# Optimization experiments

Hardware: AMD Instinct MI355X
Metric: run time of the kernel (lower is better)

Reference implementation:

```python
import jax, jax.numpy as jnp
import numpy as np

EPS = 1e-5  # BatchNorm eps

def gcn_conv(x, src, dst, deg, dinv, W, b):
    # PyG GCNConv: out = D^{-1/2}(A+I)D^{-1/2} X W + b
    N = x.shape[0]
    xw = x @ W                               # [N, F_out]
    norm = dinv[src] * dinv[dst]             # [E]
    agg = jax.ops.segment_sum(xw[src] * norm[:, None], dst, num_segments=N)
    agg = agg + xw * (1.0 / deg)[:, None]    # self-loop term: deg^-1/2 * deg^-1/2
    return agg + b

def bn(x, g, b, m, v):
    # inference-mode BatchNorm1d over features
    return (x - m) * jax.lax.rsqrt(v + EPS) * g + b

def setup_inputs() -> dict:
    key = jax.random.key(0)
    N, E, F_in, C = 100000, 1600000, 128, 16
    dims = [F_in, 64, 128, 64, 32, C]
    ks = jax.random.split(key, 64)
    inp = {}
    inp["x"] = jax.random.normal(ks[0], (N, F_in), dtype=jnp.float32)
    inp["edge_index"] = jax.random.randint(ks[1], (2, E), 0, N, dtype=jnp.int32)
    ki = 2
    for l in range(5):
        fi, fo = dims[l], dims[l + 1]
        scale = 1.0 / np.sqrt(fi)
        inp[f"w{l+1}"] = jax.random.normal(ks[ki], (fi, fo), dtype=jnp.float32) * scale; ki += 1
        inp[f"b{l+1}"] = jnp.zeros((fo,), dtype=jnp.float32)
    for l in range(4):  # BN params for layers 1..4
        fo = dims[l + 1]
        inp[f"g{l+1}"] = jnp.ones((fo,), dtype=jnp.float32)
        inp[f"be{l+1}"] = jnp.zeros((fo,), dtype=jnp.float32)
        inp[f"m{l+1}"] = jax.random.normal(ks[ki], (fo,), dtype=jnp.float32) * 0.1; ki += 1
        inp[f"v{l+1}"] = jax.random.uniform(ks[ki], (fo,), dtype=jnp.float32, minval=0.5, maxval=1.5); ki += 1
    return inp

def reference(x, edge_index,
              w1, b1, w2, b2, w3, b3, w4, b4, w5, b5,
              g1, be1, m1, v1, g2, be2, m2, v2,
              g3, be3, m3, v3, g4, be4, m4, v4):
    N = x.shape[0]
    src, dst = edge_index[0], edge_index[1]
    deg = jax.ops.segment_sum(jnp.ones(src.shape[0], x.dtype), dst, num_segments=N) + 1.0
    dinv = jax.lax.rsqrt(deg)
    h = jax.nn.relu(bn(gcn_conv(x, src, dst, deg, dinv, w1, b1), g1, be1, m1, v1))
    h = jax.nn.relu(bn(gcn_conv(h, src, dst, deg, dinv, w2, b2), g2, be2, m2, v2))
    h = jax.nn.relu(bn(gcn_conv(h, src, dst, deg, dinv, w3, b3), g3, be3, m3, v3))
    h = jax.nn.relu(bn(gcn_conv(h, src, dst, deg, dinv, w4, b4), g4, be4, m4, v4))
    return gcn_conv(h, src, dst, deg, dinv, w5, b5)
```

## Files before the change

kernel.cpp:

```cpp
#include <hip/hip_runtime.h>
#include <hip/hip_fp16.h>

#define BEPS 1e-5f
static constexpr int TPB = 256;
static constexpr int G_SC = 512;
static constexpr int BK_SHIFT = 8;
static constexpr int BK_NODES = 256;
static constexpr int KMAX = 512;

union F4H8 { float4 f4; __half2 h2[4]; };

typedef _Float16 half8 __attribute__((ext_vector_type(8)));
typedef float floatx4 __attribute__((ext_vector_type(4)));


__global__ __launch_bounds__(TPB) void k_zero_int(int* __restrict__ p, int n) {
  int i = blockIdx.x * TPB + threadIdx.x;
  if (i < n) p[i] = 0;
}

__global__ __launch_bounds__(TPB) void k_hist(const int* __restrict__ dst,
                                              int* __restrict__ histG,
                                              int* __restrict__ btot,
                                              int E, int K, int chunk) {
  __shared__ int lh[KMAX];
  int g = blockIdx.x, t = threadIdx.x;
  for (int i = t; i < KMAX; i += TPB) lh[i] = 0;
  __syncthreads();
  int e0 = g * chunk, e1 = min(E, e0 + chunk);
  for (int e = e0 + t; e < e1; e += TPB) atomicAdd(&lh[dst[e] >> BK_SHIFT], 1);
  __syncthreads();
  for (int i = t; i < K; i += TPB) {
    histG[i * G_SC + g] = lh[i];
    atomicAdd(&btot[i], lh[i]);
  }
}

__global__ __launch_bounds__(KMAX) void k_bbase(const int* __restrict__ btot,
                                                int* __restrict__ bbase, int K) {
  __shared__ int sh[KMAX];
  int t = threadIdx.x;
  int v = (t < K) ? btot[t] : 0;
  sh[t] = v;
  __syncthreads();
  for (int s = 1; s < KMAX; s <<= 1) {
    int x = sh[t];
    int y = (t >= s) ? sh[t - s] : 0;
    __syncthreads();
    sh[t] = x + y;
    __syncthreads();
  }
  if (t < K) bbase[t] = sh[t] - v;
  if (t == 0) bbase[K] = sh[K - 1];
}

__global__ __launch_bounds__(G_SC) void k_offs(const int* __restrict__ histG,
                                               const int* __restrict__ bbase,
                                               int* __restrict__ offs) {
  __shared__ int sh[G_SC];
  int b = blockIdx.x, t = threadIdx.x;
  int v = histG[b * G_SC + t];
  sh[t] = v;
  __syncthreads();
  for (int s = 1; s < G_SC; s <<= 1) {
    int x = sh[t];
    int y = (t >= s) ? sh[t - s] : 0;
    __syncthreads();
    sh[t] = x + y;
    __syncthreads();
  }
  offs[b * G_SC + t] = bbase[b] + sh[t] - v;
}

__global__ __launch_bounds__(TPB) void k_scatter(const int* __restrict__ src,
                                                 const int* __restrict__ dst,
                                                 const int* __restrict__ offs,
                                                 unsigned int* __restrict__ pairs,
                                                 int E, int K, int chunk) {
  __shared__ int cur[KMAX];
  int g = blockIdx.x, t = threadIdx.x;
  for (int i = t; i < K; i += TPB) cur[i] = offs[i * G_SC + g];
  __syncthreads();
  int e0 = g * chunk, e1 = min(E, e0 + chunk);
  for (int e = e0 + t; e < e1; e += TPB) {
    int d = dst[e];
    int b = d >> BK_SHIFT;
    int pos = atomicAdd(&cur[b], 1);
    pairs[pos] = (unsigned int)src[e] | ((unsigned int)(d & (BK_NODES - 1)) << 20);
  }
}

__global__ __launch_bounds__(TPB) void k_bucket_sort(const unsigned int* __restrict__ pairs,
                                                     const int* __restrict__ bbase,
                                                     int* __restrict__ rowptr,
                                                     int* __restrict__ colidx,
                                                     float* __restrict__ dinv,
                                                     int N, int E) {
  __shared__ int deg[BK_NODES];
  __shared__ int sh[BK_NODES];
  int b = blockIdx.x, t = threadIdx.x;
  int base = bbase[b], end = bbase[b + 1];
  int n0 = b << BK_SHIFT;
  int nNodes = min(BK_NODES, N - n0);
  deg[t] = 0;
  __syncthreads();
  for (int e = base + t; e < end; e += TPB) atomicAdd(&deg[pairs[e] >> 20], 1);
  __syncthreads();
  int v = deg[t];
  sh[t] = v;
  __syncthreads();
  for (int s = 1; s < TPB; s <<= 1) {
    int x = sh[t];
    int y = (t >= s) ? sh[t - s] : 0;
    __syncthreads();
    sh[t] = x + y;
    __syncthreads();
  }
  int excl = sh[t] - v;
  if (t < nNodes) {
    rowptr[n0 + t] = base + excl;
    dinv[n0 + t] = rsqrtf((float)(v + 1));
  }
  if (b == (int)gridDim.x - 1 && t == 0) rowptr[N] = E;
  __syncthreads();
  deg[t] = excl;
  __syncthreads();
  for (int e = base + t; e < end; e += TPB) {
    unsigned int p = pairs[e];
    int pos = atomicAdd(&deg[p >> 20], 1);
    colidx[base + pos] = (int)(p & 0xFFFFFu);
  }
}

__global__ __launch_bounds__(TPB) void k_packW(const float* __restrict__ W,
                                               _Float16* __restrict__ Wp,
                                               int K, int FO) {
  int i = blockIdx.x * TPB + threadIdx.x;
  if (i >= K * FO) return;
  int j = i & 7;
  int lane = (i >> 3) & 63;
  int tile = i >> 9;
  int nct = FO >> 4;
  int ct = tile % nct, kch = tile / nct;
  int k = kch * 32 + ((lane >> 4) << 3) + j;
  int n = (ct << 4) + (lane & 15);
  Wp[i] = (_Float16)W[k * FO + n];
}

template <int FI, int FO, int EPI, bool F32IN>
__global__ __launch_bounds__(TPB) void k_mgemm(const void* __restrict__ hin,
                                               const _Float16* __restrict__ Wp,
                                               const float* __restrict__ dinv,
                                               const float* __restrict__ bias,
                                               const float* __restrict__ g,
                                               const float* __restrict__ be,
                                               const float* __restrict__ m,
                                               const float* __restrict__ v,
                                               __half* __restrict__ out, int N) {
  constexpr int NCT = FO / 16;
  constexpr int NKC = FI / 32;
  __shared__ float4 Wsh[NKC * NCT * 64];
  for (int i = threadIdx.x; i < NKC * NCT * 64; i += TPB)
    Wsh[i] = reinterpret_cast<const float4*>(Wp)[i];
  __syncthreads();

  int lane = threadIdx.x & 63;
  int wv = threadIdx.x >> 6;
  int quad = lane >> 4;
  int rowBase = blockIdx.x * 64 + wv * 16;
  int rA = min(rowBase + (lane & 15), N - 1);

  floatx4 acc[NCT];
#pragma unroll
  for (int ct = 0; ct < NCT; ++ct) acc[ct] = (floatx4){0.f, 0.f, 0.f, 0.f};

#pragma unroll
  for (int kch = 0; kch < NKC; ++kch) {
    half8 a;
    if constexpr (F32IN) {
      const float4* xp = reinterpret_cast<const float4*>(hin);
      size_t idx = ((size_t)rA * FI + kch * 32 + quad * 8) >> 2;
      float4 fa = xp[idx], fb = xp[idx + 1];
      a[0] = (_Float16)fa.x; a[1] = (_Float16)fa.y; a[2] = (_Float16)fa.z; a[3] = (_Float16)fa.w;
      a[4] = (_Float16)fb.x; a[5] = (_Float16)fb.y; a[6] = (_Float16)fb.z; a[7] = (_Float16)fb.w;
    } else {
      union { float4 f4; half8 h8; } ua;
      ua.f4 = reinterpret_cast<const float4*>(hin)[((size_t)rA * FI + kch * 32 + quad * 8) >> 3];
      a = ua.h8;
    }
#pragma unroll
    for (int ct = 0; ct < NCT; ++ct) {
      union { float4 f4; half8 h8; } ub;
      ub.f4 = Wsh[(kch * NCT + ct) * 64 + lane];
      acc[ct] = __builtin_amdgcn_mfma_f32_16x16x32_f16(a, ub.h8, acc[ct], 0, 0, 0);
    }
  }

  int r0 = rowBase + quad * 4;
  if (EPI == 0) {
    float dv[4];
#pragma unroll
    for (int reg = 0; reg < 4; ++reg) dv[reg] = (r0 + reg < N) ? dinv[r0 + reg] : 0.f;
#pragma unroll
    for (int ct = 0; ct < NCT; ++ct) {
      int col = ct * 16 + (lane & 15);
#pragma unroll
      for (int reg = 0; reg < 4; ++reg) {
        int r = r0 + reg;
        if (r < N) out[(size_t)r * FO + col] = __float2half(acc[ct][reg] * dv[reg]);
      }
    }
  } else {
#pragma unroll
    for (int ct = 0; ct < NCT; ++ct) {
      int col = ct * 16 + (lane & 15);
      float sc = g[col] * rsqrtf(v[col] + BEPS);
      float bb = bias[col] - m[col];
      float ee = be[col];
#pragma unroll
      for (int reg = 0; reg < 4; ++reg) {
        int r = r0 + reg;
        if (r < N) out[(size_t)r * FO + col] = __float2half(fmaxf((acc[ct][reg] + bb) * sc + ee, 0.f));
      }
    }
  }
}

template <int F, int MODE, typename TO>
__global__ __launch_bounds__(TPB) void k_agg(const __half* __restrict__ in,
                                             const int* __restrict__ rowptr,
                                             const int* __restrict__ colidx,
                                             const float* __restrict__ dinv,
                                             const float* __restrict__ bias,
                                             const float* __restrict__ g,
                                             const float* __restrict__ be,
                                             const float* __restrict__ m,
                                             const float* __restrict__ v,
                                             TO* __restrict__ out, int N) {
  constexpr int V = F / 8;
  constexpr int NPB = TPB / V;
  int node = blockIdx.x * NPB + (int)(threadIdx.x / V);
  int lane = threadIdx.x % V;
  if (node >= N) return;
  const float4* in16 = reinterpret_cast<const float4*>(in);
  const size_t rs = F / 8;
  float acc[8];
  {
    F4H8 u;
    u.f4 = in16[(size_t)node * rs + lane];
#pragma unroll
    for (int i = 0; i < 4; ++i) {
      float2 t2 = __half22float2(u.h2[i]);
      acc[2 * i] = t2.x;
      acc[2 * i + 1] = t2.y;
    }
  }
  int e0 = rowptr[node], e1 = rowptr[node + 1];
  int e = e0;
  for (; e + 4 <= e1; e += 4) {
    int s0 = colidx[e + 0], s1 = colidx[e + 1], s2 = colidx[e + 2], s3 = colidx[e + 3];
    F4H8 u0, u1, u2, u3;
    u0.f4 = in16[(size_t)s0 * rs + lane];
    u1.f4 = in16[(size_t)s1 * rs + lane];
    u2.f4 = in16[(size_t)s2 * rs + lane];
    u3.f4 = in16[(size_t)s3 * rs + lane];
#pragma unroll
    for (int i = 0; i < 4; ++i) {
      float2 a = __half22float2(u0.h2[i]), b = __half22float2(u1.h2[i]);
      float2 c = __half22float2(u2.h2[i]), d = __half22float2(u3.h2[i]);
      acc[2 * i] += (a.x + b.x) + (c.x + d.x);
      acc[2 * i + 1] += (a.y + b.y) + (c.y + d.y);
    }
  }
  for (; e < e1; ++e) {
    F4H8 u;
    u.f4 = in16[(size_t)colidx[e] * rs + lane];
#pragma unroll
    for (int i = 0; i < 4; ++i) {
      float2 t2 = __half22float2(u.h2[i]);
      acc[2 * i] += t2.x;
      acc[2 * i + 1] += t2.y;
    }
  }
  float dv = dinv[node];
#pragma unroll
  for (int i = 0; i < 8; ++i) acc[i] *= dv;
  if (MODE == 0) {
    float4 ba = reinterpret_cast<const float4*>(bias)[lane * 2];
    float4 bb = reinterpret_cast<const float4*>(bias)[lane * 2 + 1];
    acc[0] += ba.x; acc[1] += ba.y; acc[2] += ba.z; acc[3] += ba.w;
    acc[4] += bb.x; acc[5] += bb.y; acc[6] += bb.z; acc[7] += bb.w;
  } else if (MODE == 1 || MODE == 2) {
    const float4* B = reinterpret_cast<const float4*>(bias);
    const float4* G = reinterpret_cast<const float4*>(g);
    const float4* Be = reinterpret_cast<const float4*>(be);
    const float4* M = reinterpret_cast<const float4*>(m);
    const float4* Vv = reinterpret_cast<const float4*>(v);
#pragma unroll
    for (int h = 0; h < 2; ++h) {
      float4 b4 = B[lane * 2 + h], g4 = G[lane * 2 + h], e4 = Be[lane * 2 + h];
      float4 m4 = M[lane * 2 + h], v4 = Vv[lane * 2 + h];
      float* a = acc + 4 * h;
      a[0] = fmaxf((a[0] + b4.x - m4.x) * (g4.x * rsqrtf(v4.x + BEPS)) + e4.x, 0.f);
      a[1] = fmaxf((a[1] + b4.y - m4.y) * (g4.y * rsqrtf(v4.y + BEPS)) + e4.y, 0.f);
      a[2] = fmaxf((a[2] + b4.z - m4.z) * (g4.z * rsqrtf(v4.z + BEPS)) + e4.z, 0.f);
      a[3] = fmaxf((a[3] + b4.w - m4.w) * (g4.w * rsqrtf(v4.w + BEPS)) + e4.w, 0.f);
    }
    if (MODE == 2) {
#pragma unroll
      for (int i = 0; i < 8; ++i) acc[i] *= dv;
    }
  }
  if constexpr (sizeof(TO) == 2) {
    F4H8 u;
#pragma unroll
    for (int i = 0; i < 4; ++i) u.h2[i] = __floats2half2_rn(acc[2 * i], acc[2 * i + 1]);
    reinterpret_cast<float4*>(out)[(size_t)node * rs + lane] = u.f4;
  } else {
    float4 o0 = {acc[0], acc[1], acc[2], acc[3]};
    float4 o1 = {acc[4], acc[5], acc[6], acc[7]};
    float4* op = reinterpret_cast<float4*>((float*)out + (size_t)node * F + lane * 8);
    op[0] = o0;
    op[1] = o1;
  }
}


extern "C" void kernel_launch(void* const* d_in, const int* in_sizes, int n_in,
                              void* d_out, int out_size, void* d_ws, size_t ws_size,
                              hipStream_t stream) {
  const float* x = (const float*)d_in[0];
  const int* ei = (const int*)d_in[1];
  const int N = in_sizes[0] / 128;
  const int E = in_sizes[1] / 2;
  const int* src = ei;
  const int* dst = ei + E;

  const float* w1 = (const float*)d_in[2];  const float* b1 = (const float*)d_in[3];
  const float* w2 = (const float*)d_in[4];  const float* b2 = (const float*)d_in[5];
  const float* w3 = (const float*)d_in[6];  const float* b3 = (const float*)d_in[7];
  const float* w4 = (const float*)d_in[8];  const float* b4 = (const float*)d_in[9];
  const float* w5 = (const float*)d_in[10]; const float* b5 = (const float*)d_in[11];
  const float* g1 = (const float*)d_in[12]; const float* be1 = (const float*)d_in[13];
  const float* m1 = (const float*)d_in[14]; const float* v1 = (const float*)d_in[15];
  const float* g2 = (const float*)d_in[16]; const float* be2 = (const float*)d_in[17];
  const float* m2 = (const float*)d_in[18]; const float* v2 = (const float*)d_in[19];
  const float* g3 = (const float*)d_in[20]; const float* be3 = (const float*)d_in[21];
  const float* m3 = (const float*)d_in[22]; const float* v3 = (const float*)d_in[23];
  const float* g4 = (const float*)d_in[24]; const float* be4 = (const float*)d_in[25];
  const float* m4 = (const float*)d_in[26]; const float* v4 = (const float*)d_in[27];
  float* out = (float*)d_out;

  char* ws = (char*)d_ws;
  size_t off = 0;
  auto alloc = [&](size_t bytes) -> void* {
    void* p = ws + off;
    off += (bytes + 255) & ~(size_t)255;
    return p;
  };
  float*        dinv   = (float*)alloc((size_t)N * 4);
  int*          rowptr = (int*)alloc((size_t)(N + 1) * 4);
  int*          colidx = (int*)alloc((size_t)E * 4);
  unsigned int* pairs  = (unsigned int*)alloc((size_t)E * 4);
  int*          histG  = (int*)alloc((size_t)KMAX * G_SC * 4);
  int*          offs   = (int*)alloc((size_t)KMAX * G_SC * 4);
  int*          btot   = (int*)alloc(KMAX * 4);
  int*          bbase  = (int*)alloc((KMAX + 1) * 4);
  _Float16*     wp1    = (_Float16*)alloc(128 * 64 * 2);
  _Float16*     wp2    = (_Float16*)alloc(64 * 128 * 2);
  _Float16*     wp3    = (_Float16*)alloc(128 * 64 * 2);
  _Float16*     wp4    = (_Float16*)alloc(64 * 32 * 2);
  _Float16*     wp5    = (_Float16*)alloc(32 * 16 * 2);
  __half*       bufA   = (__half*)alloc((size_t)N * 128 * 2);
  __half*       bufB   = (__half*)alloc((size_t)N * 128 * 2);
  (void)ws_size; (void)n_in; (void)out_size;

  const int K = (N + BK_NODES - 1) >> BK_SHIFT;
  const int chunk = (E + G_SC - 1) / G_SC;

  k_zero_int<<<2, TPB, 0, stream>>>(btot, KMAX);
  k_hist<<<G_SC, TPB, 0, stream>>>(dst, histG, btot, E, K, chunk);
  k_bbase<<<1, KMAX, 0, stream>>>(btot, bbase, K);
  k_offs<<<K, G_SC, 0, stream>>>(histG, bbase, offs);
  k_scatter<<<G_SC, TPB, 0, stream>>>(src, dst, offs, pairs, E, K, chunk);
  k_bucket_sort<<<K, TPB, 0, stream>>>(pairs, bbase, rowptr, colidx, dinv, N, E);

  k_packW<<<(128 * 64 + TPB - 1) / TPB, TPB, 0, stream>>>(w1, wp1, 128, 64);
  k_packW<<<(64 * 128 + TPB - 1) / TPB, TPB, 0, stream>>>(w2, wp2, 64, 128);
  k_packW<<<(128 * 64 + TPB - 1) / TPB, TPB, 0, stream>>>(w3, wp3, 128, 64);
  k_packW<<<(64 * 32 + TPB - 1) / TPB, TPB, 0, stream>>>(w4, wp4, 64, 32);
  k_packW<<<(32 * 16 + TPB - 1) / TPB, TPB, 0, stream>>>(w5, wp5, 32, 16);

  int gRow = (N + 63) / 64;
  k_mgemm<128, 64, 0, true><<<gRow, TPB, 0, stream>>>(x, wp1, dinv, nullptr, nullptr, nullptr, nullptr, nullptr, bufB, N);
  k_agg<64, 2, __half><<<(N + 31) / 32, TPB, 0, stream>>>(bufB, rowptr, colidx, dinv, b1, g1, be1, m1, v1, bufA, N);
  k_agg<64, 3, __half><<<(N + 31) / 32, TPB, 0, stream>>>(bufA, rowptr, colidx, dinv, nullptr, nullptr, nullptr, nullptr, nullptr, bufB, N);
  k_mgemm<64, 128, 1, false><<<gRow, TPB, 0, stream>>>(bufB, wp2, nullptr, b2, g2, be2, m2, v2, bufA, N);
  k_mgemm<128, 64, 0, false><<<gRow, TPB, 0, stream>>>(bufA, wp3, dinv, nullptr, nullptr, nullptr, nullptr, nullptr, bufB, N);
  k_agg<64, 1, __half><<<(N + 31) / 32, TPB, 0, stream>>>(bufB, rowptr, colidx, dinv, b3, g3, be3, m3, v3, bufA, N);
  k_mgemm<64, 32, 0, false><<<gRow, TPB, 0, stream>>>(bufA, wp4, dinv, nullptr, nullptr, nullptr, nullptr, nullptr, bufB, N);
  k_agg<32, 1, __half><<<(N + 63) / 64, TPB, 0, stream>>>(bufB, rowptr, colidx, dinv, b4, g4, be4, m4, v4, bufA, N);
  k_mgemm<32, 16, 0, false><<<gRow, TPB, 0, stream>>>(bufA, wp5, dinv, nullptr, nullptr, nullptr, nullptr, nullptr, bufB, N);
  k_agg<16, 0, float><<<(N + 127) / 128, TPB, 0, stream>>>(bufB, rowptr, colidx, dinv, b5, nullptr, nullptr, nullptr, nullptr, out, N);
}
```

Measured before the change: 389.6 us.

## Process aggregation nodes in degree-sorted order, unroll gathers by eight, merge weight packing

A degree histogram is built during CSR construction and counting-sorted into a node permutation. The permutation runs highest degree first, so each wavefront in the aggregation kernels handles nodes with similar neighbor counts and waits less on its slowest node. The aggregation loop also gains an 8-way unrolled gather to keep more loads in flight. The five weight-packing launches are merged into one. In exchange there are two extra small kernels, and per-node reads and writes follow a permuted, scattered order that loses locality.

```diff
diff --git a/kernel.cpp b/kernel.cpp
--- a/kernel.cpp
+++ b/kernel.cpp
@@ -95,6 +95,7 @@
                                                      int* __restrict__ rowptr,
                                                      int* __restrict__ colidx,
                                                      float* __restrict__ dinv,
+                                                     int* __restrict__ dhist,
                                                      int N, int E) {
   __shared__ int deg[BK_NODES];
   __shared__ int sh[BK_NODES];
@@ -120,6 +121,7 @@
   if (t < nNodes) {
     rowptr[n0 + t] = base + excl;
     dinv[n0 + t] = rsqrtf((float)(v + 1));
+    atomicAdd(&dhist[min(v, 63)], 1);
   }
   if (b == (int)gridDim.x - 1 && t == 0) rowptr[N] = E;
   __syncthreads();
@@ -132,19 +134,50 @@
   }
 }
 
-__global__ __launch_bounds__(TPB) void k_packW(const float* __restrict__ W,
-                                               _Float16* __restrict__ Wp,
-                                               int K, int FO) {
+__global__ __launch_bounds__(64) void k_degbase(const int* __restrict__ dhist,
+                                                int* __restrict__ dcur) {
+  __shared__ int sh[64];
+  int t = threadIdx.x;
+  sh[t] = dhist[t];
+  __syncthreads();
+  if (t == 0) {
+    int acc = 0;
+    for (int d = 63; d >= 0; --d) { int c = sh[d]; sh[d] = acc; acc += c; }
+  }
+  __syncthreads();
+  dcur[t] = sh[t];
+}
+
+__global__ __launch_bounds__(TPB) void k_degscatter(const int* __restrict__ rowptr,
+                                                    int* __restrict__ dcur,
+                                                    int* __restrict__ order, int N) {
   int i = blockIdx.x * TPB + threadIdx.x;
-  if (i >= K * FO) return;
-  int j = i & 7;
-  int lane = (i >> 3) & 63;
-  int tile = i >> 9;
-  int nct = FO >> 4;
-  int ct = tile % nct, kch = tile / nct;
+  if (i >= N) return;
+  int d = min(rowptr[i + 1] - rowptr[i], 63);
+  int pos = atomicAdd(&dcur[d], 1);
+  order[pos] = i;
+}
+
+__device__ inline void packone(const float* __restrict__ W, _Float16* __restrict__ Wp,
+                               int i, int FO) {
+  int j = i & 7, lane = (i >> 3) & 63, tile = i >> 9;
+  int nct = FO >> 4, ct = tile % nct, kch = tile / nct;
   int k = kch * 32 + ((lane >> 4) << 3) + j;
   int n = (ct << 4) + (lane & 15);
   Wp[i] = (_Float16)W[k * FO + n];
+}
+
+__global__ __launch_bounds__(TPB) void k_packAll(const float* w1, _Float16* p1,
+                                                 const float* w2, _Float16* p2,
+                                                 const float* w3, _Float16* p3,
+                                                 const float* w4, _Float16* p4,
+                                                 const float* w5, _Float16* p5) {
+  int i = blockIdx.x * TPB + threadIdx.x;
+  if (i < 8192) packone(w1, p1, i, 64);
+  else if (i < 16384) packone(w2, p2, i - 8192, 128);
+  else if (i < 24576) packone(w3, p3, i - 16384, 64);
+  else if (i < 26624) packone(w4, p4, i - 24576, 32);
+  else if (i < 27136) packone(w5, p5, i - 26624, 16);
 }
 
 template <int FI, int FO, int EPI, bool F32IN>
@@ -230,6 +263,7 @@
 __global__ __launch_bounds__(TPB) void k_agg(const __half* __restrict__ in,
                                              const int* __restrict__ rowptr,
                                              const int* __restrict__ colidx,
+                                             const int* __restrict__ order,
                                              const float* __restrict__ dinv,
                                              const float* __restrict__ bias,
                                              const float* __restrict__ g,
@@ -239,9 +273,10 @@
                                              TO* __restrict__ out, int N) {
   constexpr int V = F / 8;
   constexpr int NPB = TPB / V;
-  int node = blockIdx.x * NPB + (int)(threadIdx.x / V);
+  int gidx = blockIdx.x * NPB + (int)(threadIdx.x / V);
   int lane = threadIdx.x % V;
-  if (node >= N) return;
+  if (gidx >= N) return;
+  int node = order[gidx];
   const float4* in16 = reinterpret_cast<const float4*>(in);
   const size_t rs = F / 8;
   float acc[8];
@@ -257,6 +292,23 @@
   }
   int e0 = rowptr[node], e1 = rowptr[node + 1];
   int e = e0;
+  for (; e + 8 <= e1; e += 8) {
+    int s[8];
+#pragma unroll
+    for (int q = 0; q < 8; ++q) s[q] = colidx[e + q];
+    F4H8 u[8];
+#pragma unroll
+    for (int q = 0; q < 8; ++q) u[q].f4 = in16[(size_t)s[q] * rs + lane];
+#pragma unroll
+    for (int q = 0; q < 8; ++q) {
+#pragma unroll
+      for (int i = 0; i < 4; ++i) {
+        float2 t2 = __half22float2(u[q].h2[i]);
+        acc[2 * i] += t2.x;
+        acc[2 * i + 1] += t2.y;
+      }
+    }
+  }
   for (; e + 4 <= e1; e += 4) {
     int s0 = colidx[e + 0], s1 = colidx[e + 1], s2 = colidx[e + 2], s3 = colidx[e + 3];
     F4H8 u0, u1, u2, u3;
@@ -365,6 +417,9 @@
   int*          histG  = (int*)alloc((size_t)KMAX * G_SC * 4);
   int*          offs   = (int*)alloc((size_t)KMAX * G_SC * 4);
   int*          btot   = (int*)alloc(KMAX * 4);
+  int*          dhist  = (int*)alloc(64 * 4);
+  int*          dcur   = (int*)alloc(64 * 4);
+  int*          order  = (int*)alloc((size_t)N * 4);
   int*          bbase  = (int*)alloc((KMAX + 1) * 4);
   _Float16*     wp1    = (_Float16*)alloc(128 * 64 * 2);
   _Float16*     wp2    = (_Float16*)alloc(64 * 128 * 2);
@@ -378,28 +433,26 @@
   const int K = (N + BK_NODES - 1) >> BK_SHIFT;
   const int chunk = (E + G_SC - 1) / G_SC;
 
-  k_zero_int<<<2, TPB, 0, stream>>>(btot, KMAX);
+  k_zero_int<<<3, TPB, 0, stream>>>(btot, KMAX + 64);
   k_hist<<<G_SC, TPB, 0, stream>>>(dst, histG, btot, E, K, chunk);
   k_bbase<<<1, KMAX, 0, stream>>>(btot, bbase, K);
   k_offs<<<K, G_SC, 0, stream>>>(histG, bbase, offs);
   k_scatter<<<G_SC, TPB, 0, stream>>>(src, dst, offs, pairs, E, K, chunk);
-  k_bucket_sort<<<K, TPB, 0, stream>>>(pairs, bbase, rowptr, colidx, dinv, N, E);
-
-  k_packW<<<(128 * 64 + TPB - 1) / TPB, TPB, 0, stream>>>(w1, wp1, 128, 64);
-  k_packW<<<(64 * 128 + TPB - 1) / TPB, TPB, 0, stream>>>(w2, wp2, 64, 128);
-  k_packW<<<(128 * 64 + TPB - 1) / TPB, TPB, 0, stream>>>(w3, wp3, 128, 64);
-  k_packW<<<(64 * 32 + TPB - 1) / TPB, TPB, 0, stream>>>(w4, wp4, 64, 32);
-  k_packW<<<(32 * 16 + TPB - 1) / TPB, TPB, 0, stream>>>(w5, wp5, 32, 16);
+  k_bucket_sort<<<K, TPB, 0, stream>>>(pairs, bbase, rowptr, colidx, dinv, dhist, N, E);
+  k_degbase<<<1, 64, 0, stream>>>(dhist, dcur);
+  k_degscatter<<<(N + TPB - 1) / TPB, TPB, 0, stream>>>(rowptr, dcur, order, N);
+
+  k_packAll<<<(27136 + TPB - 1) / TPB, TPB, 0, stream>>>(w1, wp1, w2, wp2, w3, wp3, w4, wp4, w5, wp5);
 
   int gRow = (N + 63) / 64;
   k_mgemm<128, 64, 0, true><<<gRow, TPB, 0, stream>>>(x, wp1, dinv, nullptr, nullptr, nullptr, nullptr, nullptr, bufB, N);
-  k_agg<64, 2, __half><<<(N + 31) / 32, TPB, 0, stream>>>(bufB, rowptr, colidx, dinv, b1, g1, be1, m1, v1, bufA, N);
-  k_agg<64, 3, __half><<<(N + 31) / 32, TPB, 0, stream>>>(bufA, rowptr, colidx, dinv, nullptr, nullptr, nullptr, nullptr, nullptr, bufB, N);
+  k_agg<64, 2, __half><<<(N + 31) / 32, TPB, 0, stream>>>(bufB, rowptr, colidx, order, dinv, b1, g1, be1, m1, v1, bufA, N);
+  k_agg<64, 3, __half><<<(N + 31) / 32, TPB, 0, stream>>>(bufA, rowptr, colidx, order, dinv, nullptr, nullptr, nullptr, nullptr, nullptr, bufB, N);
   k_mgemm<64, 128, 1, false><<<gRow, TPB, 0, stream>>>(bufB, wp2, nullptr, b2, g2, be2, m2, v2, bufA, N);
   k_mgemm<128, 64, 0, false><<<gRow, TPB, 0, stream>>>(bufA, wp3, dinv, nullptr, nullptr, nullptr, nullptr, nullptr, bufB, N);
-  k_agg<64, 1, __half><<<(N + 31) / 32, TPB, 0, stream>>>(bufB, rowptr, colidx, dinv, b3, g3, be3, m3, v3, bufA, N);
+  k_agg<64, 1, __half><<<(N + 31) / 32, TPB, 0, stream>>>(bufB, rowptr, colidx, order, dinv, b3, g3, be3, m3, v3, bufA, N);
   k_mgemm<64, 32, 0, false><<<gRow, TPB, 0, stream>>>(bufA, wp4, dinv, nullptr, nullptr, nullptr, nullptr, nullptr, bufB, N);
-  k_agg<32, 1, __half><<<(N + 63) / 64, TPB, 0, stream>>>(bufB, rowptr, colidx, dinv, b4, g4, be4, m4, v4, bufA, N);
+  k_agg<32, 1, __half><<<(N + 63) / 64, TPB, 0, stream>>>(bufB, rowptr, colidx, order, dinv, b4, g4, be4, m4, v4, bufA, N);
   k_mgemm<32, 16, 0, false><<<gRow, TPB, 0, stream>>>(bufA, wp5, dinv, nullptr, nullptr, nullptr, nullptr, nullptr, bufB, N);
-  k_agg<16, 0, float><<<(N + 127) / 128, TPB, 0, stream>>>(bufB, rowptr, colidx, dinv, b5, nullptr, nullptr, nullptr, nullptr, out, N);
-}
+  k_agg<16, 0, float><<<(N + 127) / 128, TPB, 0, stream>>>(bufB, rowptr, colidx, order, dinv, b5, nullptr, nullptr, nullptr, nullptr, out, N);
+}
```

Result: slower. 912.2 us (+134.1%).

## Pad CSR rows to multiples of eight and vectorize neighbor gathers

Applied to the files above, without the earlier changes.

The bucket sort now builds a padded CSR. Each node's neighbor list is rounded up to a multiple of 8 using a dummy index N, which points at a zeroed row, and a per-node rowend array is added. The aggregation loop loads column indices as int4 pairs, prefetches the next eight, and issues eight gathers per iteration with no remainder loop. The GEMM row guards are dropped because the buffers are over-allocated, and the five weight-pack launches are merged into one kernel that also zeroes the padding row. In exchange, extra gathers hit the dummy row, and correctness depends on row N staying zero in each buffer the aggregation reads.

```diff
diff --git a/kernel.cpp b/kernel.cpp
--- a/kernel.cpp
+++ b/kernel.cpp
@@ -7,6 +7,7 @@
 static constexpr int BK_SHIFT = 8;
 static constexpr int BK_NODES = 256;
 static constexpr int KMAX = 512;
+static constexpr int BK_SLACK = 2048;
 
 union F4H8 { float4 f4; __half2 h2[4]; };
 
@@ -93,21 +94,23 @@
 __global__ __launch_bounds__(TPB) void k_bucket_sort(const unsigned int* __restrict__ pairs,
                                                      const int* __restrict__ bbase,
                                                      int* __restrict__ rowptr,
+                                                     int* __restrict__ rowend,
                                                      int* __restrict__ colidx,
                                                      float* __restrict__ dinv,
                                                      int N, int E) {
-  __shared__ int deg[BK_NODES];
+  __shared__ int cur[BK_NODES];
   __shared__ int sh[BK_NODES];
   int b = blockIdx.x, t = threadIdx.x;
   int base = bbase[b], end = bbase[b + 1];
   int n0 = b << BK_SHIFT;
   int nNodes = min(BK_NODES, N - n0);
-  deg[t] = 0;
-  __syncthreads();
-  for (int e = base + t; e < end; e += TPB) atomicAdd(&deg[pairs[e] >> 20], 1);
-  __syncthreads();
-  int v = deg[t];
-  sh[t] = v;
+  cur[t] = 0;
+  __syncthreads();
+  for (int e = base + t; e < end; e += TPB) atomicAdd(&cur[pairs[e] >> 20], 1);
+  __syncthreads();
+  int v = cur[t];
+  int pd = (v + 7) & ~7;
+  sh[t] = pd;
   __syncthreads();
   for (int s = 1; s < TPB; s <<= 1) {
     int x = sh[t];
@@ -116,35 +119,49 @@
     sh[t] = x + y;
     __syncthreads();
   }
-  int excl = sh[t] - v;
+  int Bb = (base + b * BK_SLACK + 7) & ~7;
+  int start = Bb + (sh[t] - pd);
   if (t < nNodes) {
-    rowptr[n0 + t] = base + excl;
+    rowptr[n0 + t] = start;
+    rowend[n0 + t] = start + pd;
     dinv[n0 + t] = rsqrtf((float)(v + 1));
-  }
-  if (b == (int)gridDim.x - 1 && t == 0) rowptr[N] = E;
-  __syncthreads();
-  deg[t] = excl;
+    for (int i = start + v; i < start + pd; ++i) colidx[i] = N;
+  }
+  __syncthreads();
+  cur[t] = start;
   __syncthreads();
   for (int e = base + t; e < end; e += TPB) {
     unsigned int p = pairs[e];
-    int pos = atomicAdd(&deg[p >> 20], 1);
-    colidx[base + pos] = (int)(p & 0xFFFFFu);
-  }
-}
-
-__global__ __launch_bounds__(TPB) void k_packW(const float* __restrict__ W,
-                                               _Float16* __restrict__ Wp,
-                                               int K, int FO) {
-  int i = blockIdx.x * TPB + threadIdx.x;
-  if (i >= K * FO) return;
-  int j = i & 7;
-  int lane = (i >> 3) & 63;
-  int tile = i >> 9;
-  int nct = FO >> 4;
-  int ct = tile % nct, kch = tile / nct;
+    int pos = atomicAdd(&cur[p >> 20], 1);
+    colidx[pos] = (int)(p & 0xFFFFFu);
+  }
+}
+
+__device__ inline void packone(const float* __restrict__ W, _Float16* __restrict__ Wp,
+                               int i, int FO) {
+  int j = i & 7, lane = (i >> 3) & 63, tile = i >> 9;
+  int nct = FO >> 4, ct = tile % nct, kch = tile / nct;
   int k = kch * 32 + ((lane >> 4) << 3) + j;
   int n = (ct << 4) + (lane & 15);
   Wp[i] = (_Float16)W[k * FO + n];
+}
+
+__global__ __launch_bounds__(TPB) void k_packAll(const float* w1, _Float16* p1,
+                                                 const float* w2, _Float16* p2,
+                                                 const float* w3, _Float16* p3,
+                                                 const float* w4, _Float16* p4,
+                                                 const float* w5, _Float16* p5,
+                                                 __half* bufA, int N) {
+  int i = blockIdx.x * TPB + threadIdx.x;
+  if (i < 8192) packone(w1, p1, i, 64);
+  else if (i < 16384) packone(w2, p2, i - 8192, 128);
+  else if (i < 24576) packone(w3, p3, i - 16384, 64);
+  else if (i < 26624) packone(w4, p4, i - 24576, 32);
+  else if (i < 27136) packone(w5, p5, i - 26624, 16);
+  else if (i < 27144) {
+    float4 z = {0.f, 0.f, 0.f, 0.f};
+    reinterpret_cast<float4*>(bufA + (size_t)64 * N)[i - 27136] = z;
+  }
 }
 
 template <int FI, int FO, int EPI, bool F32IN>
@@ -207,7 +224,7 @@
 #pragma unroll
       for (int reg = 0; reg < 4; ++reg) {
         int r = r0 + reg;
-        if (r < N) out[(size_t)r * FO + col] = __float2half(acc[ct][reg] * dv[reg]);
+        out[(size_t)r * FO + col] = __float2half(acc[ct][reg] * dv[reg]);
       }
     }
   } else {
@@ -220,7 +237,7 @@
 #pragma unroll
       for (int reg = 0; reg < 4; ++reg) {
         int r = r0 + reg;
-        if (r < N) out[(size_t)r * FO + col] = __float2half(fmaxf((acc[ct][reg] + bb) * sc + ee, 0.f));
+        out[(size_t)r * FO + col] = __float2half(fmaxf((acc[ct][reg] + bb) * sc + ee, 0.f));
       }
     }
   }
@@ -229,6 +246,7 @@
 template <int F, int MODE, typename TO>
 __global__ __launch_bounds__(TPB) void k_agg(const __half* __restrict__ in,
                                              const int* __restrict__ rowptr,
+                                             const int* __restrict__ rowend,
                                              const int* __restrict__ colidx,
                                              const float* __restrict__ dinv,
                                              const float* __restrict__ bias,
@@ -255,32 +273,38 @@
       acc[2 * i + 1] = t2.y;
     }
   }
-  int e0 = rowptr[node], e1 = rowptr[node + 1];
-  int e = e0;
-  for (; e + 4 <= e1; e += 4) {
-    int s0 = colidx[e + 0], s1 = colidx[e + 1], s2 = colidx[e + 2], s3 = colidx[e + 3];
-    F4H8 u0, u1, u2, u3;
-    u0.f4 = in16[(size_t)s0 * rs + lane];
-    u1.f4 = in16[(size_t)s1 * rs + lane];
-    u2.f4 = in16[(size_t)s2 * rs + lane];
-    u3.f4 = in16[(size_t)s3 * rs + lane];
-#pragma unroll
-    for (int i = 0; i < 4; ++i) {
-      float2 a = __half22float2(u0.h2[i]), b = __half22float2(u1.h2[i]);
-      float2 c = __half22float2(u2.h2[i]), d = __half22float2(u3.h2[i]);
-      acc[2 * i] += (a.x + b.x) + (c.x + d.x);
-      acc[2 * i + 1] += (a.y + b.y) + (c.y + d.y);
-    }
-  }
-  for (; e < e1; ++e) {
-    F4H8 u;
-    u.f4 = in16[(size_t)colidx[e] * rs + lane];
-#pragma unroll
-    for (int i = 0; i < 4; ++i) {
-      float2 t2 = __half22float2(u.h2[i]);
-      acc[2 * i] += t2.x;
-      acc[2 * i + 1] += t2.y;
-    }
+  int e0 = rowptr[node], e1 = rowend[node];
+  int4 c0, c1;
+  if (e0 < e1) {
+    c0 = *reinterpret_cast<const int4*>(colidx + e0);
+    c1 = *reinterpret_cast<const int4*>(colidx + e0 + 4);
+  }
+  for (int e = e0; e < e1; e += 8) {
+    int4 n0, n1;
+    int en = e + 8;
+    if (en < e1) {
+      n0 = *reinterpret_cast<const int4*>(colidx + en);
+      n1 = *reinterpret_cast<const int4*>(colidx + en + 4);
+    }
+    F4H8 u[8];
+    u[0].f4 = in16[(size_t)c0.x * rs + lane];
+    u[1].f4 = in16[(size_t)c0.y * rs + lane];
+    u[2].f4 = in16[(size_t)c0.z * rs + lane];
+    u[3].f4 = in16[(size_t)c0.w * rs + lane];
+    u[4].f4 = in16[(size_t)c1.x * rs + lane];
+    u[5].f4 = in16[(size_t)c1.y * rs + lane];
+    u[6].f4 = in16[(size_t)c1.z * rs + lane];
+    u[7].f4 = in16[(size_t)c1.w * rs + lane];
+#pragma unroll
+    for (int q = 0; q < 8; ++q) {
+#pragma unroll
+      for (int i = 0; i < 4; ++i) {
+        float2 t2 = __half22float2(u[q].h2[i]);
+        acc[2 * i] += t2.x;
+        acc[2 * i + 1] += t2.y;
+      }
+    }
+    c0 = n0; c1 = n1;
   }
   float dv = dinv[node];
 #pragma unroll
@@ -358,9 +382,11 @@
     off += (bytes + 255) & ~(size_t)255;
     return p;
   };
+  const int K = (N + BK_NODES - 1) >> BK_SHIFT;
   float*        dinv   = (float*)alloc((size_t)N * 4);
-  int*          rowptr = (int*)alloc((size_t)(N + 1) * 4);
-  int*          colidx = (int*)alloc((size_t)E * 4);
+  int*          rowptr = (int*)alloc((size_t)N * 4);
+  int*          rowend = (int*)alloc((size_t)N * 4);
+  int*          colidx = (int*)alloc(((size_t)E + (size_t)(K + 1) * BK_SLACK) * 4);
   unsigned int* pairs  = (unsigned int*)alloc((size_t)E * 4);
   int*          histG  = (int*)alloc((size_t)KMAX * G_SC * 4);
   int*          offs   = (int*)alloc((size_t)KMAX * G_SC * 4);
@@ -371,11 +397,10 @@
   _Float16*     wp3    = (_Float16*)alloc(128 * 64 * 2);
   _Float16*     wp4    = (_Float16*)alloc(64 * 32 * 2);
   _Float16*     wp5    = (_Float16*)alloc(32 * 16 * 2);
-  __half*       bufA   = (__half*)alloc((size_t)N * 128 * 2);
-  __half*       bufB   = (__half*)alloc((size_t)N * 128 * 2);
+  __half*       bufA   = (__half*)alloc((size_t)(N + 64) * 128 * 2);
+  __half*       bufB   = (__half*)alloc((size_t)(N + 64) * 128 * 2);
   (void)ws_size; (void)n_in; (void)out_size;
 
-  const int K = (N + BK_NODES - 1) >> BK_SHIFT;
   const int chunk = (E + G_SC - 1) / G_SC;
 
   k_zero_int<<<2, TPB, 0, stream>>>(btot, KMAX);
@@ -383,23 +408,19 @@
   k_bbase<<<1, KMAX, 0, stream>>>(btot, bbase, K);
   k_offs<<<K, G_SC, 0, stream>>>(histG, bbase, offs);
   k_scatter<<<G_SC, TPB, 0, stream>>>(src, dst, offs, pairs, E, K, chunk);
-  k_bucket_sort<<<K, TPB, 0, stream>>>(pairs, bbase, rowptr, colidx, dinv, N, E);
-
-  k_packW<<<(128 * 64 + TPB - 1) / TPB, TPB, 0, stream>>>(w1, wp1, 128, 64);
-  k_packW<<<(64 * 128 + TPB - 1) / TPB, TPB, 0, stream>>>(w2, wp2, 64, 128);
-  k_packW<<<(128 * 64 + TPB - 1) / TPB, TPB, 0, stream>>>(w3, wp3, 128, 64);
-  k_packW<<<(64 * 32 + TPB - 1) / TPB, TPB, 0, stream>>>(w4, wp4, 64, 32);
-  k_packW<<<(32 * 16 + TPB - 1) / TPB, TPB, 0, stream>>>(w5, wp5, 32, 16);
+  k_bucket_sort<<<K, TPB, 0, stream>>>(pairs, bbase, rowptr, rowend, colidx, dinv, N, E);
+
+  k_packAll<<<(27144 + TPB - 1) / TPB, TPB, 0, stream>>>(w1, wp1, w2, wp2, w3, wp3, w4, wp4, w5, wp5, bufA, N);
 
   int gRow = (N + 63) / 64;
   k_mgemm<128, 64, 0, true><<<gRow, TPB, 0, stream>>>(x, wp1, dinv, nullptr, nullptr, nullptr, nullptr, nullptr, bufB, N);
-  k_agg<64, 2, __half><<<(N + 31) / 32, TPB, 0, stream>>>(bufB, rowptr, colidx, dinv, b1, g1, be1, m1, v1, bufA, N);
-  k_agg<64, 3, __half><<<(N + 31) / 32, TPB, 0, stream>>>(bufA, rowptr, colidx, dinv, nullptr, nullptr, nullptr, nullptr, nullptr, bufB, N);
+  k_agg<64, 2, __half><<<(N + 31) / 32, TPB, 0, stream>>>(bufB, rowptr, rowend, colidx, dinv, b1, g1, be1, m1, v1, bufA, N);
+  k_agg<64, 3, __half><<<(N + 31) / 32, TPB, 0, stream>>>(bufA, rowptr, rowend, colidx, dinv, nullptr, nullptr, nullptr, nullptr, nullptr, bufB, N);
   k_mgemm<64, 128, 1, false><<<gRow, TPB, 0, stream>>>(bufB, wp2, nullptr, b2, g2, be2, m2, v2, bufA, N);
   k_mgemm<128, 64, 0, false><<<gRow, TPB, 0, stream>>>(bufA, wp3, dinv, nullptr, nullptr, nullptr, nullptr, nullptr, bufB, N);
-  k_agg<64, 1, __half><<<(N + 31) / 32, TPB, 0, stream>>>(bufB, rowptr, colidx, dinv, b3, g3, be3, m3, v3, bufA, N);
+  k_agg<64, 1, __half><<<(N + 31) / 32, TPB, 0, stream>>>(bufB, rowptr, rowend, colidx, dinv, b3, g3, be3, m3, v3, bufA, N);
   k_mgemm<64, 32, 0, false><<<gRow, TPB, 0, stream>>>(bufA, wp4, dinv, nullptr, nullptr, nullptr, nullptr, nullptr, bufB, N);
-  k_agg<32, 1, __half><<<(N + 63) / 64, TPB, 0, stream>>>(bufB, rowptr, colidx, dinv, b4, g4, be4, m4, v4, bufA, N);
+  k_agg<32, 1, __half><<<(N + 63) / 64, TPB, 0, stream>>>(bufB, rowptr, rowend, colidx, dinv, b4, g4, be4, m4, v4, bufA, N);
   k_mgemm<32, 16, 0, false><<<gRow, TPB, 0, stream>>>(bufA, wp5, dinv, nullptr, nullptr, nullptr, nullptr, nullptr, bufB, N);
-  k_agg<16, 0, float><<<(N + 127) / 128, TPB, 0, stream>>>(bufB, rowptr, colidx, dinv, b5, nullptr, nullptr, nullptr, nullptr, out, N);
-}
+  k_agg<16, 0, float><<<(N + 127) / 128, TPB, 0, stream>>>(bufB, rowptr, rowend, colidx, dinv, b5, nullptr, nullptr, nullptr, nullptr, out, N);
+}
```

New measurement: 363.8 us. 6.6% less time.
